# Performance work log

Hardware: AMD Instinct MI355X
Metric: run time of the kernel (lower is better)

Reference implementation:

```python
import jax, jax.numpy as jnp
import numpy as np

B, T, D = 4, 2048, 512
H, HS = 8, 64            # n_head, head_size
E, K = 8, 2              # num_experts, top_k
CAP = int(B * T * K / E * 1.0)  # expert capacity = 2048
EPS = 1e-5


def setup_inputs() -> dict:
    key = jax.random.key(0)
    ks = jax.random.split(key, 16)
    s = lambda k, shp, fan: jax.random.normal(k, shp, jnp.float32) * (fan ** -0.5)
    return {
        "x": jax.random.normal(ks[0], (B, T, D), jnp.float32),
        "ln1_g": jnp.ones((D,), jnp.float32), "ln1_b": jnp.zeros((D,), jnp.float32),
        "Wq": s(ks[1], (H, D, HS), D), "Wk": s(ks[2], (H, D, HS), D), "Wv": s(ks[3], (H, D, HS), D),
        "Wo": s(ks[4], (D, D), D), "bo": jnp.zeros((D,), jnp.float32),
        "ln2_g": jnp.ones((D,), jnp.float32), "ln2_b": jnp.zeros((D,), jnp.float32),
        "Wg": s(ks[5], (D, E), D), "bg": jnp.zeros((E,), jnp.float32),
        "Wn": s(ks[6], (D, E), D), "bn": jnp.zeros((E,), jnp.float32),
        "W1": s(ks[7], (E, D, 4 * D), D), "b1": jnp.zeros((E, 4 * D), jnp.float32),
        "W2": s(ks[8], (E, 4 * D, D), 4 * D), "b2": jnp.zeros((E, D), jnp.float32),
    }


def _ln(x, g, b):
    m = jnp.mean(x, -1, keepdims=True)
    v = jnp.var(x, -1, keepdims=True)
    return (x - m) * jax.lax.rsqrt(v + EPS) * g + b


def _attn(h, Wq, Wk, Wv, Wo, bo):
    q = jnp.einsum('btd,hde->bhte', h, Wq)
    k = jnp.einsum('btd,hde->bhte', h, Wk)
    v = jnp.einsum('btd,hde->bhte', h, Wv)
    # NOTE: source scales by C**-0.5 with C = n_embed (not head_size)
    wei = jnp.einsum('bhte,bhse->bhts', q, k) * (D ** -0.5)
    causal = jnp.tril(jnp.ones((T, T), bool))
    wei = jnp.where(causal, wei, -jnp.inf)
    wei = jax.nn.softmax(wei, axis=-1)
    out = jnp.einsum('bhts,bhse->bhte', wei, v)              # [B,H,T,HS]
    out = out.transpose(0, 2, 1, 3).reshape(B, T, D)          # concat heads
    return out @ Wo + bo


def _moe(h, Wg, bg, Wn, bn, W1, b1, W2, b2):
    logits = h @ Wg + bg
    noise_logits = h @ Wn + bn
    noise = jax.random.normal(jax.random.key(42), logits.shape, logits.dtype) * jax.nn.softplus(noise_logits)
    noisy = logits + noise
    vals, idx = jax.lax.top_k(noisy, K)                       # [B,T,K]
    # softmax over -inf-masked sparse logits == softmax over top-k values, scattered
    gates = (jax.nn.softmax(vals, -1)[..., None] * jax.nn.one_hot(idx, E, dtype=h.dtype)).sum(-2)  # [B,T,E]
    flat_x = h.reshape(-1, D)
    flat_g = gates.reshape(-1, E)
    flat_idx = idx.reshape(-1, K)
    N = flat_x.shape[0]
    mask = (flat_idx[None] == jnp.arange(E)[:, None, None]).any(-1)   # [E,N]
    rank = jnp.cumsum(mask, axis=1) - 1
    keep = mask & (rank < CAP)                                 # first CAP tokens per expert
    slot = jnp.where(keep, rank, CAP)
    tok = jnp.arange(N, dtype=jnp.int32)

    def build(s, kp):
        buf = jnp.zeros(CAP + 1, jnp.int32).at[s].set(tok)
        vb = jnp.zeros(CAP + 1, bool).at[s].set(kp)
        return buf[:CAP], vb[:CAP]

    idx_buf, valid = jax.vmap(build)(slot, keep)               # [E,CAP]
    xg = flat_x[idx_buf]                                       # [E,CAP,D]
    mid = jax.nn.relu(jnp.einsum('ecd,edf->ecf', xg, W1) + b1[:, None, :])
    out = jnp.einsum('ecf,efd->ecd', mid, W2) + b2[:, None, :]
    gate_sel = flat_g[idx_buf, jnp.arange(E)[:, None]]         # [E,CAP]
    w = out * (gate_sel * valid.astype(h.dtype))[..., None]
    upd = jnp.zeros_like(flat_x).at[idx_buf.reshape(-1)].add(w.reshape(-1, D))
    return upd.reshape(h.shape)


def reference(x, ln1_g, ln1_b, Wq, Wk, Wv, Wo, bo, ln2_g, ln2_b,
              Wg, bg, Wn, bn, W1, b1, W2, b2):
    x = x + _attn(_ln(x, ln1_g, ln1_b), Wq, Wk, Wv, Wo, bo)
    x = x + _moe(_ln(x, ln2_g, ln2_b), Wg, bg, Wn, bn, W1, b1, W2, b2)
    return x
```

## Files before the change

kernel.cpp:

```cpp
#include <hip/hip_runtime.h>
#include <math.h>

#define TSEQ 2048
#define DD   512
#define NH   8
#define HSZ  64
#define NE   8
#define NTOK 8192
#define CAPK 2048
#define FF   2048

typedef __bf16 bf16x8 __attribute__((ext_vector_type(8)));
typedef float  f32x4  __attribute__((ext_vector_type(4)));
typedef unsigned int u32;
typedef u32 u32x2 __attribute__((ext_vector_type(2)));
typedef short s16x4 __attribute__((ext_vector_type(4)));

#define WAITVM(N) asm volatile("s_waitcnt vmcnt(" #N ")" ::: "memory")

__device__ __forceinline__ void gload16(const void* g, void* l){
  __builtin_amdgcn_global_load_lds((const __attribute__((address_space(1))) u32*)g,
                                   (__attribute__((address_space(3))) u32*)l, 16, 0, 0);
}

__device__ __forceinline__ u32 pkbf(float a, float b){
  unsigned short ua = __builtin_bit_cast(unsigned short, (__bf16)a);
  unsigned short ub = __builtin_bit_cast(unsigned short, (__bf16)b);
  return (u32)ua | ((u32)ub << 16);
}

__device__ __forceinline__ s16x4 mk4(u32 a, u32 b){
  u32x2 t; t[0] = a; t[1] = b;
  return __builtin_bit_cast(s16x4, t);
}

__device__ __forceinline__ unsigned rotl32(unsigned x, int r){ return (x<<r)|(x>>(32-r)); }

__device__ __forceinline__ void threefry2x32(unsigned c0, unsigned c1, unsigned &o0, unsigned &o1){
  const unsigned k0 = 0u, k1 = 42u;
  const unsigned k2 = k0 ^ k1 ^ 0x1BD11BDAu;
  unsigned x0 = c0 + k0, x1 = c1 + k1;
#define TFR(rot) { x0 += x1; x1 = rotl32(x1, rot); x1 ^= x0; }
  TFR(13) TFR(15) TFR(26) TFR(6)   x0 += k1; x1 += k2 + 1u;
  TFR(17) TFR(29) TFR(16) TFR(24)  x0 += k2; x1 += k0 + 2u;
  TFR(13) TFR(15) TFR(26) TFR(6)   x0 += k0; x1 += k1 + 3u;
  TFR(17) TFR(29) TFR(16) TFR(24)  x0 += k1; x1 += k2 + 4u;
  TFR(13) TFR(15) TFR(26) TFR(6)   x0 += k2; x1 += k0 + 5u;
#undef TFR
  o0 = x0; o1 = x1;
}

__device__ __forceinline__ float erfinv_f(float x){
  float w = -log1pf(-x*x);
  float p;
  if (w < 5.0f){
    w -= 2.5f;
    p = 2.81022636e-08f;
    p = fmaf(p,w, 3.43273939e-07f);
    p = fmaf(p,w,-3.5233877e-06f);
    p = fmaf(p,w,-4.39150654e-06f);
    p = fmaf(p,w, 0.00021858087f);
    p = fmaf(p,w,-0.00125372503f);
    p = fmaf(p,w,-0.00417768164f);
    p = fmaf(p,w, 0.246640727f);
    p = fmaf(p,w, 1.50140941f);
  } else {
    w = sqrtf(w) - 3.0f;
    p = -0.000200214257f;
    p = fmaf(p,w, 0.000100950558f);
    p = fmaf(p,w, 0.00134934322f);
    p = fmaf(p,w,-0.00367342844f);
    p = fmaf(p,w, 0.00573950773f);
    p = fmaf(p,w,-0.0076224613f);
    p = fmaf(p,w, 0.00943887047f);
    p = fmaf(p,w, 1.00167406f);
    p = fmaf(p,w, 2.83297682f);
  }
  return p * x;
}

__global__ __launch_bounds__(256) void prep_kernel(
    const float* __restrict__ x, const float* __restrict__ ln1g, const float* __restrict__ ln1b,
    __bf16* __restrict__ h1hi, __bf16* __restrict__ h1lo,
    const float* __restrict__ Wq, const float* __restrict__ Wk, const float* __restrict__ Wv,
    __bf16* __restrict__ Bqh, __bf16* __restrict__ Bql,
    const float* __restrict__ Wo, __bf16* __restrict__ WoTh, __bf16* __restrict__ WoTl)
{
  __shared__ float t[64][65];
  int blk = blockIdx.x;
  int tid = threadIdx.x;
  if (blk < 2048){
    int row  = blk*4 + (tid >> 6);
    int lane = tid & 63;
    const float* xr = x + (size_t)row*DD;
    float4 a = *(const float4*)(xr + lane*4);
    float4 c = *(const float4*)(xr + 256 + lane*4);
    float s  = a.x+a.y+a.z+a.w + c.x+c.y+c.z+c.w;
    float ss = a.x*a.x+a.y*a.y+a.z*a.z+a.w*a.w + c.x*c.x+c.y*c.y+c.z*c.z+c.w*c.w;
    #pragma unroll
    for (int off = 32; off; off >>= 1){ s += __shfl_xor(s, off); ss += __shfl_xor(ss, off); }
    float m   = s * (1.0f/DD);
    float var = ss * (1.0f/DD) - m*m;
    float r   = 1.0f / sqrtf(var + 1e-5f);
    float4 g1 = *(const float4*)(ln1g + lane*4);
    float4 b1 = *(const float4*)(ln1b + lane*4);
    float4 g2 = *(const float4*)(ln1g + 256 + lane*4);
    float4 b2 = *(const float4*)(ln1b + 256 + lane*4);
    float f1[4], f2[4];
    f1[0]=(a.x-m)*r*g1.x+b1.x; f1[1]=(a.y-m)*r*g1.y+b1.y; f1[2]=(a.z-m)*r*g1.z+b1.z; f1[3]=(a.w-m)*r*g1.w+b1.w;
    f2[0]=(c.x-m)*r*g2.x+b2.x; f2[1]=(c.y-m)*r*g2.y+b2.y; f2[2]=(c.z-m)*r*g2.z+b2.z; f2[3]=(c.w-m)*r*g2.w+b2.w;
    __bf16 h1v[4] __attribute__((aligned(8))), l1v[4] __attribute__((aligned(8)));
    __bf16 h2v[4] __attribute__((aligned(8))), l2v[4] __attribute__((aligned(8)));
    #pragma unroll
    for (int j = 0; j < 4; ++j){
      __bf16 hb = (__bf16)f1[j]; h1v[j]=hb; l1v[j]=(__bf16)(f1[j]-(float)hb);
      __bf16 hc = (__bf16)f2[j]; h2v[j]=hc; l2v[j]=(__bf16)(f2[j]-(float)hc);
    }
    size_t base = (size_t)row*DD + lane*4;
    *(uint2*)(h1hi + base)       = *(const uint2*)h1v;
    *(uint2*)(h1lo + base)       = *(const uint2*)l1v;
    *(uint2*)(h1hi + base + 256) = *(const uint2*)h2v;
    *(uint2*)(h1lo + base + 256) = *(const uint2*)l2v;
  } else if (blk < 2240){
    int bx = blk - 2048;
    int kt = (bx & 7) * 64;
    int z  = bx >> 3;
    int sel = z >> 3, hh = z & 7;
    const float* W = (sel==0 ? Wq : (sel==1 ? Wk : Wv)) + (size_t)hh*DD*HSZ;
    int r = tid>>2, c0 = (tid&3)*16;
    #pragma unroll
    for (int j = 0; j < 16; j += 4){
      float4 v = *(const float4*)&W[(size_t)(kt+r)*HSZ + c0 + j];
      t[r][c0+j]=v.x; t[r][c0+j+1]=v.y; t[r][c0+j+2]=v.z; t[r][c0+j+3]=v.w;
    }
    __syncthreads();
    __bf16 hb[16] __attribute__((aligned(32)));
    __bf16 lb[16] __attribute__((aligned(32)));
    #pragma unroll
    for (int j = 0; j < 16; ++j){
      float f = t[c0+j][r];
      __bf16 h = (__bf16)f; hb[j]=h; lb[j]=(__bf16)(f-(float)h);
    }
    size_t off = (size_t)(z*64 + r)*512 + kt + c0;
    *(uint4*)(Bqh+off) = ((const uint4*)hb)[0]; *(uint4*)(Bqh+off+8) = ((const uint4*)hb)[1];
    *(uint4*)(Bql+off) = ((const uint4*)lb)[0]; *(uint4*)(Bql+off+8) = ((const uint4*)lb)[1];
  } else {
    int bx = blk - 2240;
    int nt = (bx & 7) * 64, mt = (bx >> 3) * 64;
    int r = tid>>2, c0 = (tid&3)*16;
    #pragma unroll
    for (int j = 0; j < 16; j += 4){
      float4 v = *(const float4*)&Wo[(size_t)(mt+r)*DD + nt + c0 + j];
      t[r][c0+j]=v.x; t[r][c0+j+1]=v.y; t[r][c0+j+2]=v.z; t[r][c0+j+3]=v.w;
    }
    __syncthreads();
    __bf16 hb[16] __attribute__((aligned(32)));
    __bf16 lb[16] __attribute__((aligned(32)));
    #pragma unroll
    for (int j = 0; j < 16; ++j){
      float f = t[c0+j][r];
      __bf16 h = (__bf16)f; hb[j]=h; lb[j]=(__bf16)(f-(float)h);
    }
    size_t off = (size_t)(nt + r)*DD + mt + c0;
    *(uint4*)(WoTh+off) = ((const uint4*)hb)[0]; *(uint4*)(WoTh+off+8) = ((const uint4*)hb)[1];
    *(uint4*)(WoTl+off) = ((const uint4*)lb)[0]; *(uint4*)(WoTl+off+8) = ((const uint4*)lb)[1];
  }
}

template<int BIAS, int RES>
__global__ __launch_bounds__(256) void gemm_mfma3(
    const __bf16* __restrict__ Ahi, const __bf16* __restrict__ Alo,
    const __bf16* __restrict__ Bhi, const __bf16* __restrict__ Blo,
    const float* __restrict__ bias, const float* __restrict__ res,
    float* __restrict__ C, int M, int N, int K)
{
  __shared__ __bf16 AsH[2][4096];
  __shared__ __bf16 AsL[2][4096];
  __shared__ __bf16 BsH[2][4096];
  __shared__ __bf16 BsL[2][4096];
  int m0 = blockIdx.y*128, n0 = blockIdx.x*128;
  int tid = threadIdx.x;
  int w = tid>>6, l = tid&63;
  int wm = w>>1, wn = w&1;
  int srow = w*32 + (l>>2);
  int skb  = (l&3)<<4;
  const char* agh = (const char*)(Ahi + (size_t)(m0+srow)*K) + skb;
  const char* agl = (const char*)(Alo + (size_t)(m0+srow)*K) + skb;
  const char* bgh = (const char*)(Bhi + (size_t)(n0+srow)*K) + skb;
  const char* bgl = (const char*)(Blo + (size_t)(n0+srow)*K) + skb;
  size_t r16 = (size_t)16*K*sizeof(__bf16);

  f32x4 acc[4][4] = {};
  int rl = l & 15, kh = l >> 4;
  const __bf16* abh = &AsH[0][(wm*64 + rl)*32 + kh*8];
  const __bf16* abl = &AsL[0][(wm*64 + rl)*32 + kh*8];
  const __bf16* bbh = &BsH[0][(wn*64 + rl)*32 + kh*8];
  const __bf16* bbl = &BsL[0][(wn*64 + rl)*32 + kh*8];

  auto STAGE = [&](int bb, int kt){
    size_t o = (size_t)kt*64;
    gload16(agh+o,     &AsH[bb][w*1024]);
    gload16(agh+o+r16, &AsH[bb][w*1024+512]);
    gload16(agl+o,     &AsL[bb][w*1024]);
    gload16(agl+o+r16, &AsL[bb][w*1024+512]);
    gload16(bgh+o,     &BsH[bb][w*1024]);
    gload16(bgh+o+r16, &BsH[bb][w*1024+512]);
    gload16(bgl+o,     &BsL[bb][w*1024]);
    gload16(bgl+o+r16, &BsL[bb][w*1024+512]);
  };

  int nkt = K >> 5;
  STAGE(0, 0);
  for (int kt = 0; kt < nkt; ++kt){
    int bb = kt & 1;
    if (kt + 1 < nkt){ STAGE(bb^1, kt+1); WAITVM(8); }
    else             { WAITVM(0); }
    __builtin_amdgcn_s_barrier();
    bf16x8 afh[4], afl[4], bfh[4], bfl[4];
    #pragma unroll
    for (int i = 0; i < 4; ++i){
      afh[i] = *(const bf16x8*)(abh + bb*4096 + i*512);
      afl[i] = *(const bf16x8*)(abl + bb*4096 + i*512);
      bfh[i] = *(const bf16x8*)(bbh + bb*4096 + i*512);
      bfl[i] = *(const bf16x8*)(bbl + bb*4096 + i*512);
    }
    #pragma unroll
    for (int fm = 0; fm < 4; ++fm)
      #pragma unroll
      for (int fn = 0; fn < 4; ++fn){
        acc[fm][fn] = __builtin_amdgcn_mfma_f32_16x16x32_bf16(afh[fm], bfl[fn], acc[fm][fn], 0, 0, 0);
        acc[fm][fn] = __builtin_amdgcn_mfma_f32_16x16x32_bf16(afl[fm], bfh[fn], acc[fm][fn], 0, 0, 0);
        acc[fm][fn] = __builtin_amdgcn_mfma_f32_16x16x32_bf16(afh[fm], bfh[fn], acc[fm][fn], 0, 0, 0);
      }
    __builtin_amdgcn_s_barrier();
  }

  int ccol = l & 15, cr = (l >> 4) * 4;
  #pragma unroll
  for (int fn = 0; fn < 4; ++fn){
    int n = n0 + wn*64 + fn*16 + ccol;
    float bv = BIAS ? bias[n] : 0.0f;
    #pragma unroll
    for (int fm = 0; fm < 4; ++fm){
      int mb = m0 + wm*64 + fm*16 + cr;
      #pragma unroll
      for (int r = 0; r < 4; ++r){
        float v = acc[fm][fn][r] + bv;
        if (RES) v += res[(size_t)(mb+r)*N + n];
        C[(size_t)(mb+r)*N + n] = v;
      }
    }
  }
}

template<int STORE_BF16, int RELU, int GATHER, int LOGN, int EBITS>
__global__ __launch_bounds__(256) void gemm_mfma(
    const __bf16* __restrict__ A, const __bf16* __restrict__ Bt,
    const float* __restrict__ bias, void* __restrict__ Cv,
    const int* __restrict__ idxb, int M, int N, int K)
{
  __shared__ __bf16 Asl[2][4096];
  __shared__ __bf16 Bsl[2][4096];
  int flat = blockIdx.x;
  int e = flat & ((1<<EBITS)-1);
  int tile = flat >> EBITS;
  int n0 = (tile & ((1<<LOGN)-1)) * 128;
  int m0 = (tile >> LOGN) * 128;
  const __bf16* Be = Bt + (size_t)e*N*K;
  const float*  be = bias + (size_t)e*N;
  int tid = threadIdx.x;
  int w = tid>>6, l = tid&63;
  int wm = w>>1, wn = w&1;
  int srow = w*32 + (l>>2);
  int skb  = (l&3)<<4;
  const char* ag;
  if (GATHER){
    int tok = idxb[e*CAPK + m0 + srow];
    ag = (const char*)(A + (size_t)tok*K) + skb;
  } else {
    ag = (const char*)(A + (size_t)e*M*K + (size_t)(m0 + srow)*K) + skb;
  }
  const char* bg = (const char*)(Be + (size_t)(n0 + srow)*K) + skb;
  size_t r16;
  if (GATHER){
    int tok2 = idxb[e*CAPK + m0 + srow + 16];
    r16 = (size_t)((const char*)(A + (size_t)tok2*K) + skb - ag);
  } else {
    r16 = (size_t)16*K*sizeof(__bf16);
  }

  f32x4 acc[4][4] = {};
  int rl = l & 15, kh = l >> 4;
  const __bf16* abase = &Asl[0][(wm*64 + rl)*32 + kh*8];
  const __bf16* bbase = &Bsl[0][(wn*64 + rl)*32 + kh*8];

  size_t br16 = (size_t)16*K*sizeof(__bf16);
  auto STAGE = [&](int bb, int kt){
    size_t o = (size_t)kt*64;
    gload16(ag+o,      &Asl[bb][w*1024]);
    gload16(ag+o+r16,  &Asl[bb][w*1024+512]);
    gload16(bg+o,      &Bsl[bb][w*1024]);
    gload16(bg+o+br16, &Bsl[bb][w*1024+512]);
  };

  int nkt = K >> 5;
  STAGE(0, 0);
  for (int kt = 0; kt < nkt; ++kt){
    int bb = kt & 1;
    if (kt + 1 < nkt){ STAGE(bb^1, kt+1); WAITVM(4); }
    else             { WAITVM(0); }
    __builtin_amdgcn_s_barrier();
    bf16x8 af[4], bf[4];
    #pragma unroll
    for (int i = 0; i < 4; ++i){
      af[i] = *(const bf16x8*)(abase + bb*4096 + i*512);
      bf[i] = *(const bf16x8*)(bbase + bb*4096 + i*512);
    }
    #pragma unroll
    for (int fm = 0; fm < 4; ++fm)
      #pragma unroll
      for (int fn = 0; fn < 4; ++fn)
        acc[fm][fn] = __builtin_amdgcn_mfma_f32_16x16x32_bf16(af[fm], bf[fn], acc[fm][fn], 0, 0, 0);
    __builtin_amdgcn_s_barrier();
  }

  int ccol = l & 15, cr = (l >> 4) * 4;
  char* Ce = (char*)Cv + (size_t)e*M*N*(STORE_BF16 ? 2 : 4);
  #pragma unroll
  for (int fn = 0; fn < 4; ++fn){
    int n = n0 + wn*64 + fn*16 + ccol;
    float bv = be[n];
    #pragma unroll
    for (int fm = 0; fm < 4; ++fm){
      int mb = m0 + wm*64 + fm*16 + cr;
      #pragma unroll
      for (int r = 0; r < 4; ++r){
        float v = acc[fm][fn][r] + bv;
        if (RELU) v = fmaxf(v, 0.f);
        if (STORE_BF16) ((__bf16*)Ce)[(size_t)(mb+r)*N + n] = (__bf16)v;
        else            ((float*)Ce)[(size_t)(mb+r)*N + n] = v;
      }
    }
  }
}

__global__ __launch_bounds__(256) void transp_conv2(const float* __restrict__ W1,
    const float* __restrict__ W2, __bf16* __restrict__ d1, __bf16* __restrict__ d2)
{
  __shared__ __bf16 t[64][72];
  int e = blockIdx.z;
  int id = blockIdx.x;
  const float* s; __bf16* d; int Ms, Ns, mt, nt;
  if (id < 256){ s = W1; d = d1; Ms = DD; Ns = FF; nt = (id&31)*64; mt = (id>>5)*64; }
  else { int i2 = id-256; s = W2; d = d2; Ms = FF; Ns = DD; nt = (i2&7)*64; mt = (i2>>3)*64; }
  s += (size_t)e*Ms*Ns;
  d += (size_t)e*Ms*Ns;
  int tid = threadIdx.x;
  int r = tid>>2, c0 = (tid&3)*16;
  #pragma unroll
  for (int j = 0; j < 16; j += 4){
    float4 v = *(const float4*)&s[(size_t)(mt+r)*Ns + nt + c0 + j];
    t[r][c0+j]   = (__bf16)v.x; t[r][c0+j+1] = (__bf16)v.y;
    t[r][c0+j+2] = (__bf16)v.z; t[r][c0+j+3] = (__bf16)v.w;
  }
  __syncthreads();
  __bf16 tmp[16] __attribute__((aligned(32)));
  #pragma unroll
  for (int j = 0; j < 16; ++j) tmp[j] = t[c0+j][r];
  uint4* dp = (uint4*)&d[(size_t)(nt+r)*Ms + mt + c0];
  dp[0] = ((const uint4*)tmp)[0];
  dp[1] = ((const uint4*)tmp)[1];
}

__global__ __launch_bounds__(256) void convert_kv(const float* __restrict__ qkv,
    __bf16* __restrict__ khi, __bf16* __restrict__ klo,
    __bf16* __restrict__ vthi, __bf16* __restrict__ vtlo)
{
  int t0 = blockIdx.x*64;
  int bh = blockIdx.y;
  int b = bh >> 3, h = bh & 7;
  int tid = threadIdx.x;
  {
    int r = tid >> 2, e0 = (tid & 3) * 16;
    const float* src = qkv + ((size_t)(b*TSEQ + t0 + r))*1536 + 512 + h*64 + e0;
    __bf16 hi[16] __attribute__((aligned(16)));
    __bf16 lo[16] __attribute__((aligned(16)));
    #pragma unroll
    for (int j = 0; j < 16; j += 4){
      float4 v = *(const float4*)(src + j);
      float f[4] = {v.x, v.y, v.z, v.w};
      #pragma unroll
      for (int q = 0; q < 4; ++q){
        __bf16 hb = (__bf16)f[q];
        hi[j+q] = hb; lo[j+q] = (__bf16)(f[q] - (float)hb);
      }
    }
    size_t off = ((size_t)(bh*TSEQ + t0 + r))*64 + e0;
    *(uint4*)(khi + off)     = ((const uint4*)hi)[0];
    *(uint4*)(khi + off + 8) = ((const uint4*)hi)[1];
    *(uint4*)(klo + off)     = ((const uint4*)lo)[0];
    *(uint4*)(klo + off + 8) = ((const uint4*)lo)[1];
  }
  {
    int key0 = (tid & 15) * 4, e0 = (tid >> 4) * 4;
    float4 v[4];
    #pragma unroll
    for (int j = 0; j < 4; ++j)
      v[j] = *(const float4*)(qkv + ((size_t)(b*TSEQ + t0 + key0 + j))*1536 + 1024 + h*64 + e0);
    float col[4][4];
    col[0][0]=v[0].x; col[0][1]=v[1].x; col[0][2]=v[2].x; col[0][3]=v[3].x;
    col[1][0]=v[0].y; col[1][1]=v[1].y; col[1][2]=v[2].y; col[1][3]=v[3].y;
    col[2][0]=v[0].z; col[2][1]=v[1].z; col[2][2]=v[2].z; col[2][3]=v[3].z;
    col[3][0]=v[0].w; col[3][1]=v[1].w; col[3][2]=v[2].w; col[3][3]=v[3].w;
    #pragma unroll
    for (int kk = 0; kk < 4; ++kk){
      __bf16 hi[4] __attribute__((aligned(8)));
      __bf16 lo[4] __attribute__((aligned(8)));
      #pragma unroll
      for (int j = 0; j < 4; ++j){
        __bf16 hb = (__bf16)col[kk][j];
        hi[j] = hb; lo[j] = (__bf16)(col[kk][j] - (float)hb);
      }
      size_t off = ((size_t)(bh*64 + e0 + kk))*TSEQ + t0 + key0;
      *(uint2*)(vthi + off) = *(const uint2*)hi;
      *(uint2*)(vtlo + off) = *(const uint2*)lo;
    }
  }
}

__global__ __launch_bounds__(512) void attn_mfma(const float* __restrict__ qkv,
    const __bf16* __restrict__ khi_g, const __bf16* __restrict__ klo_g,
    const __bf16* __restrict__ vthi_g, const __bf16* __restrict__ vtlo_g,
    __bf16* __restrict__ ahi, __bf16* __restrict__ alo)
{
  extern __shared__ __align__(16) char ldsbuf[];
  int bh = blockIdx.x;
  int qtA = blockIdx.y, qtB = 15 - qtA;
  int b = bh >> 3, h = bh & 7;
  int tid = threadIdx.x;
  int w = tid >> 6, l = tid & 63;
  int g = l >> 4, r = l & 15;
  const float qsc = 0.04419417382415922f * 1.4426950408889634f;

  int qb[2]; qb[0] = qtA*128 + w*16; qb[1] = qtB*128 + (7-w)*16;
  int kdiag[2]; kdiag[0] = qtA; kdiag[1] = qtB;

  bf16x8 qhi[2][2], qlo[2][2];
  #pragma unroll
  for (int qf = 0; qf < 2; ++qf)
    #pragma unroll
    for (int ks = 0; ks < 2; ++ks){
      const float* src = qkv + ((size_t)(b*TSEQ + qb[qf] + r))*1536 + h*64 + ks*32 + g*8;
      float4 v0 = *(const float4*)src;
      float4 v1 = *(const float4*)(src + 4);
      float f[8] = {v0.x,v0.y,v0.z,v0.w,v1.x,v1.y,v1.z,v1.w};
      bf16x8 hi, lo;
      #pragma unroll
      for (int i = 0; i < 8; ++i){
        float fs = f[i] * qsc;
        __bf16 hb = (__bf16)fs;
        hi[i] = hb; lo[i] = (__bf16)(fs - (float)hb);
      }
      qhi[qf][ks] = hi; qlo[qf][ks] = lo;
    }

  f32x4 ot[4][2] = {};
  float m_r[2] = {-INFINITY, -INFINITY};
  float l_r[2] = {0.f, 0.f};

  int nkt = qtB + 1;
  size_t kbase = (size_t)bh*TSEQ*64;
  size_t vbase = (size_t)bh*64*TSEQ;

  auto STAGE = [&](int buf, int kt){
    int row = tid >> 3, cc = tid & 7;
    char* base = ldsbuf + buf*65536 + (w << 10);
    #pragma unroll
    for (int p = 0; p < 2; ++p){
      int krow = p*64 + row;
      int ksw = (cc ^ (krow & 7)) * 8;
      gload16(khi_g + kbase + (size_t)(kt*128 + krow)*64 + ksw, base + p*8192);
      gload16(klo_g + kbase + (size_t)(kt*128 + krow)*64 + ksw, base + 16384 + p*8192);
      int vch = p*8 + cc;
      int vsw = ((vch ^ (row & 7)) & 15) * 8;
      gload16(vthi_g + vbase + (size_t)row*TSEQ + kt*128 + vsw, base + 32768 + p*8192);
      gload16(vtlo_g + vbase + (size_t)row*TSEQ + kt*128 + vsw, base + 49152 + p*8192);
    }
  };

  STAGE(0, 0);

  for (int kt = 0; kt < nkt; ++kt){
    int buf = kt & 1;
    if (kt + 1 < nkt){ STAGE(buf ^ 1, kt + 1); WAITVM(8); }
    else             { WAITVM(0); }
    __builtin_amdgcn_s_barrier();

    bool act[2];
    act[0] = (kt <= kdiag[0]);
    act[1] = true;

    const char* K0 = ldsbuf + buf*65536;
    const char* K1 = K0 + 16384;
    const char* V0 = K0 + 32768;
    const char* V1 = K0 + 49152;

    f32x4 s[8][2] = {};
    #pragma unroll
    for (int kf = 0; kf < 8; ++kf){
      int rowk = kf*16 + r;
      int rsw = (rowk & 7) << 4;
      #pragma unroll
      for (int ks = 0; ks < 2; ++ks){
        int off = rowk*128 + ((((ks*4 + g) << 4)) ^ rsw);
        bf16x8 khf = *(const bf16x8*)(K0 + off);
        bf16x8 klf = *(const bf16x8*)(K1 + off);
        #pragma unroll
        for (int qf = 0; qf < 2; ++qf){
          if (act[qf]){
            s[kf][qf] = __builtin_amdgcn_mfma_f32_16x16x32_bf16(khf, qlo[qf][ks], s[kf][qf], 0,0,0);
            s[kf][qf] = __builtin_amdgcn_mfma_f32_16x16x32_bf16(klf, qhi[qf][ks], s[kf][qf], 0,0,0);
            s[kf][qf] = __builtin_amdgcn_mfma_f32_16x16x32_bf16(khf, qhi[qf][ks], s[kf][qf], 0,0,0);
          }
        }
      }
    }

    #pragma unroll
    for (int qf = 0; qf < 2; ++qf){
      if (act[qf]){
        int q = qb[qf] + r;
        float mx = -INFINITY;
        if (kt == kdiag[qf]){
          #pragma unroll
          for (int kf = 0; kf < 8; ++kf)
            #pragma unroll
            for (int e = 0; e < 4; ++e){
              int key = kt*128 + kf*16 + g*4 + e;
              float sv = (key <= q) ? s[kf][qf][e] : -INFINITY;
              s[kf][qf][e] = sv;
              mx = fmaxf(mx, sv);
            }
        } else {
          #pragma unroll
          for (int kf = 0; kf < 8; ++kf)
            #pragma unroll
            for (int e = 0; e < 4; ++e)
              mx = fmaxf(mx, s[kf][qf][e]);
        }
        mx = fmaxf(mx, __shfl_xor(mx, 16));
        mx = fmaxf(mx, __shfl_xor(mx, 32));
        if (__any(mx > m_r[qf])){
          float mn = fmaxf(m_r[qf], mx);
          float fj = exp2f(m_r[qf] - mn);
          m_r[qf] = mn;
          l_r[qf] *= fj;
          #pragma unroll
          for (int ef = 0; ef < 4; ++ef)
            #pragma unroll
            for (int e = 0; e < 4; ++e)
              ot[ef][qf][e] *= fj;
        }
        float ts = 0.f;
        #pragma unroll
        for (int kf = 0; kf < 8; ++kf)
          #pragma unroll
          for (int e = 0; e < 4; ++e){
            float pv = exp2f(s[kf][qf][e] - m_r[qf]);
            s[kf][qf][e] = pv; ts += pv;
          }
        ts += __shfl_xor(ts, 16); ts += __shfl_xor(ts, 32);
        l_r[qf] += ts;
      }
    }

    #pragma unroll
    for (int kf = 0; kf < 8; ++kf){
      u32 PH[2][2], PL[2][2];
      #pragma unroll
      for (int qf = 0; qf < 2; ++qf){
        if (act[qf]){
          float p0 = s[kf][qf][0], p1 = s[kf][qf][1], p2 = s[kf][qf][2], p3 = s[kf][qf][3];
          __bf16 h0=(__bf16)p0, h1=(__bf16)p1, h2=(__bf16)p2, h3=(__bf16)p3;
          PH[qf][0] = pkbf(p0, p1);
          PH[qf][1] = pkbf(p2, p3);
          PL[qf][0] = pkbf(p0-(float)h0, p1-(float)h1);
          PL[qf][1] = pkbf(p2-(float)h2, p3-(float)h3);
        }
      }
      int chunk = 2*kf + (g>>1);
      int pb = (chunk >> 3) << 13;
      int cl = chunk & 7;
      #pragma unroll
      for (int ef = 0; ef < 4; ++ef){
        int rowv = ef*16 + r;
        int off = pb + rowv*128 + ((cl ^ (rowv & 7)) << 4) + (g&1)*8;
        s16x4 vh = *(const s16x4*)(V0 + off);
        s16x4 vl = *(const s16x4*)(V1 + off);
        #pragma unroll
        for (int qf = 0; qf < 2; ++qf){
          if (act[qf]){
            s16x4 ph = mk4(PH[qf][0], PH[qf][1]);
            s16x4 pl = mk4(PL[qf][0], PL[qf][1]);
            ot[ef][qf] = __builtin_amdgcn_mfma_f32_16x16x16bf16_1k(vh, pl, ot[ef][qf], 0,0,0);
            ot[ef][qf] = __builtin_amdgcn_mfma_f32_16x16x16bf16_1k(vl, ph, ot[ef][qf], 0,0,0);
            ot[ef][qf] = __builtin_amdgcn_mfma_f32_16x16x16bf16_1k(vh, ph, ot[ef][qf], 0,0,0);
          }
        }
      }
    }
    __builtin_amdgcn_s_barrier();
  }

  float* Osh = (float*)ldsbuf;
  #pragma unroll
  for (int qf = 0; qf < 2; ++qf){
    float inv = 1.0f / l_r[qf];
    int qloc = (qf ? (7-w) : w)*16 + r;
    #pragma unroll
    for (int ef = 0; ef < 4; ++ef)
      #pragma unroll
      for (int e = 0; e < 4; ++e)
        Osh[qloc*68 + ef*16 + g*4 + e] = ot[ef][qf][e] * inv;
    __syncthreads();
    {
      int qt = qf ? qtB : qtA;
      int q = tid >> 2, e0 = (tid & 3)*16;
      const float* srow = Osh + q*68 + e0;
      size_t base = ((size_t)(b*TSEQ + qt*128 + q))*DD + h*64 + e0;
      #pragma unroll
      for (int j = 0; j < 4; ++j){
        float4 v = *(const float4*)(srow + j*4);
        float f[4] = {v.x, v.y, v.z, v.w};
        __bf16 hb[4] __attribute__((aligned(8)));
        __bf16 lb[4] __attribute__((aligned(8)));
        #pragma unroll
        for (int q2 = 0; q2 < 4; ++q2){
          __bf16 h2b = (__bf16)f[q2];
          hb[q2] = h2b; lb[q2] = (__bf16)(f[q2] - (float)h2b);
        }
        *(uint2*)(ahi + base + j*4) = *(const uint2*)hb;
        *(uint2*)(alo + base + j*4) = *(const uint2*)lb;
      }
    }
    __syncthreads();
  }
}

__global__ __launch_bounds__(256) void routerln_kernel(const float* __restrict__ x1,
    const float* __restrict__ gw, const float* __restrict__ bw,
    const float* __restrict__ Wg, const float* __restrict__ bg,
    const float* __restrict__ Wn, const float* __restrict__ bn,
    __bf16* __restrict__ h2b,
    int* __restrict__ idx0, int* __restrict__ idx1,
    float* __restrict__ g0, float* __restrict__ g1)
{
  int wid = threadIdx.x >> 6, lane = threadIdx.x & 63;
  int tok = blockIdx.x*4 + wid;
  const float* xr = x1 + (size_t)tok*DD;
  float4 a = *(const float4*)(xr + lane*4);
  float4 c = *(const float4*)(xr + 256 + lane*4);
  float s  = a.x+a.y+a.z+a.w + c.x+c.y+c.z+c.w;
  float ss = a.x*a.x+a.y*a.y+a.z*a.z+a.w*a.w + c.x*c.x+c.y*c.y+c.z*c.z+c.w*c.w;
  #pragma unroll
  for (int off = 32; off; off >>= 1){ s += __shfl_xor(s, off); ss += __shfl_xor(ss, off); }
  float m   = s * (1.0f/DD);
  float var = ss * (1.0f/DD) - m*m;
  float rr  = 1.0f / sqrtf(var + 1e-5f);
  float4 g1v = *(const float4*)(gw + lane*4);
  float4 b1v = *(const float4*)(bw + lane*4);
  float4 g2v = *(const float4*)(gw + 256 + lane*4);
  float4 b2v = *(const float4*)(bw + 256 + lane*4);
  float f1[4], f2[4];
  f1[0]=(a.x-m)*rr*g1v.x+b1v.x; f1[1]=(a.y-m)*rr*g1v.y+b1v.y; f1[2]=(a.z-m)*rr*g1v.z+b1v.z; f1[3]=(a.w-m)*rr*g1v.w+b1v.w;
  f2[0]=(c.x-m)*rr*g2v.x+b2v.x; f2[1]=(c.y-m)*rr*g2v.y+b2v.y; f2[2]=(c.z-m)*rr*g2v.z+b2v.z; f2[3]=(c.w-m)*rr*g2v.w+b2v.w;
  {
    __bf16 h1v[4] __attribute__((aligned(8)));
    __bf16 h2v[4] __attribute__((aligned(8)));
    #pragma unroll
    for (int j = 0; j < 4; ++j){ h1v[j] = (__bf16)f1[j]; h2v[j] = (__bf16)f2[j]; }
    size_t base = (size_t)tok*DD + lane*4;
    *(uint2*)(h2b + base)       = *(const uint2*)h1v;
    *(uint2*)(h2b + base + 256) = *(const uint2*)h2v;
  }
  float ag[8] = {0,0,0,0,0,0,0,0}, an[8] = {0,0,0,0,0,0,0,0};
  int d1 = lane*4, d2 = 256 + lane*4;
  #pragma unroll
  for (int j = 0; j < 4; ++j){
    const float* wg1 = Wg + (size_t)(d1+j)*8;
    const float* wn1 = Wn + (size_t)(d1+j)*8;
    const float* wg2 = Wg + (size_t)(d2+j)*8;
    const float* wn2 = Wn + (size_t)(d2+j)*8;
    #pragma unroll
    for (int e = 0; e < 8; ++e){
      ag[e] = fmaf(f1[j], wg1[e], ag[e]); an[e] = fmaf(f1[j], wn1[e], an[e]);
      ag[e] = fmaf(f2[j], wg2[e], ag[e]); an[e] = fmaf(f2[j], wn2[e], an[e]);
    }
  }
  #pragma unroll
  for (int off = 32; off; off >>= 1){
    #pragma unroll
    for (int e = 0; e < 8; ++e){ ag[e] += __shfl_xor(ag[e], off); an[e] += __shfl_xor(an[e], off); }
  }
  __shared__ float ns[4][8];
  if (lane < 8){
    int e = lane;
    float lg = ag[e] + bg[e];
    float nl = an[e] + bn[e];
    float sp = fmaxf(nl, 0.f) + log1pf(expf(-fabsf(nl)));
    unsigned i = (unsigned)(tok*8 + e);
    unsigned r0b, r1b;
    threefry2x32(0u, i, r0b, r1b);
    unsigned bits = r0b ^ r1b;
    float f = __uint_as_float((bits >> 9) | 0x3f800000u) - 1.0f;
    float u = fmaf(f, 2.0f, -0.99999994f);
    u = fmaxf(u, -0.99999994f);
    float z = 1.41421356f * erfinv_f(u);
    ns[wid][e] = lg + z*sp;
  }
  __syncthreads();
  if (lane == 0){
    float v0 = -INFINITY; int i0 = 0;
    #pragma unroll
    for (int e = 0; e < 8; ++e){ float v = ns[wid][e]; if (v > v0){ v0 = v; i0 = e; } }
    float v1 = -INFINITY; int i1 = 0;
    #pragma unroll
    for (int e = 0; e < 8; ++e){ if (e != i0){ float v = ns[wid][e]; if (v > v1){ v1 = v; i1 = e; } } }
    float dexp = expf(v1 - v0);
    float ssum = 1.0f + dexp;
    idx0[tok] = i0; idx1[tok] = i1;
    g0[tok] = 1.0f/ssum; g1[tok] = dexp/ssum;
  }
}

__global__ __launch_bounds__(256) void route_scan(const int* __restrict__ idx0,
    const int* __restrict__ idx1, int* __restrict__ idx_buf, int* __restrict__ tok_slot)
{
  int e = blockIdx.x, tid = threadIdx.x;
  for (int i = tid; i < CAPK; i += 256) idx_buf[e*CAPK + i] = 0;
  __syncthreads();
  int base = tid * 32;
  int cnt = 0;
  for (int j = 0; j < 32; ++j){ int t = base + j; cnt += (idx0[t]==e || idx1[t]==e) ? 1 : 0; }
  __shared__ int ps[256];
  ps[tid] = cnt; __syncthreads();
  for (int off = 1; off < 256; off <<= 1){
    int add = (tid >= off) ? ps[tid - off] : 0;
    __syncthreads();
    ps[tid] += add;
    __syncthreads();
  }
  int slot = ps[tid] - cnt;
  for (int j = 0; j < 32; ++j){
    int t = base + j;
    int k = (idx0[t]==e) ? 0 : ((idx1[t]==e) ? 1 : -1);
    if (k >= 0){
      if (slot < CAPK){ idx_buf[e*CAPK + slot] = t; tok_slot[t*2 + k] = slot; }
      else            { tok_slot[t*2 + k] = -1; }
      slot++;
    }
  }
}

__global__ __launch_bounds__(128) void combine_kernel(const float* __restrict__ x1,
    const __bf16* __restrict__ eout, const int* __restrict__ idx0, const int* __restrict__ idx1,
    const float* __restrict__ g0, const float* __restrict__ g1,
    const int* __restrict__ tok_slot, float* __restrict__ outp)
{
  int n = blockIdx.x, t = threadIdx.x;
  float4 acc = *(const float4*)(x1 + (size_t)n*DD + t*4);
  #pragma unroll
  for (int k = 0; k < 2; ++k){
    int s = tok_slot[n*2 + k];
    if (s >= 0){
      int e  = (k==0) ? idx0[n] : idx1[n];
      float g = (k==0) ? g0[n] : g1[n];
      __bf16 vb[4] __attribute__((aligned(8)));
      *(uint2*)vb = *(const uint2*)(eout + ((size_t)(e*CAPK + s))*DD + t*4);
      acc.x = fmaf(g, (float)vb[0], acc.x); acc.y = fmaf(g, (float)vb[1], acc.y);
      acc.z = fmaf(g, (float)vb[2], acc.z); acc.w = fmaf(g, (float)vb[3], acc.w);
    }
  }
  *(float4*)(outp + (size_t)n*DD + t*4) = acc;
}

extern "C" void kernel_launch(void* const* d_in, const int* in_sizes, int n_in,
                              void* d_out, int out_size, void* d_ws, size_t ws_size,
                              hipStream_t stream)
{
  const float* x    = (const float*)d_in[0];
  const float* ln1g = (const float*)d_in[1];
  const float* ln1b = (const float*)d_in[2];
  const float* Wq   = (const float*)d_in[3];
  const float* Wk   = (const float*)d_in[4];
  const float* Wv   = (const float*)d_in[5];
  const float* Wo   = (const float*)d_in[6];
  const float* bo   = (const float*)d_in[7];
  const float* ln2g = (const float*)d_in[8];
  const float* ln2b = (const float*)d_in[9];
  const float* Wg   = (const float*)d_in[10];
  const float* bg   = (const float*)d_in[11];
  const float* Wn   = (const float*)d_in[12];
  const float* bn   = (const float*)d_in[13];
  const float* W1   = (const float*)d_in[14];
  const float* b1   = (const float*)d_in[15];
  const float* W2   = (const float*)d_in[16];
  const float* b2   = (const float*)d_in[17];
  float* out = (float*)d_out;
  char* ws = (char*)d_ws;
  const size_t MB = 1u << 20;

  (void)hipFuncSetAttribute((const void*)attn_mfma,
      hipFuncAttributeMaxDynamicSharedMemorySize, 131072);

  __bf16* h1hi   = (__bf16*)(ws);
  __bf16* h1lo   = (__bf16*)(ws + 8*MB);
  __bf16* attnhi = (__bf16*)(ws);
  __bf16* attnlo = (__bf16*)(ws + 8*MB);
  __bf16* h2b    = (__bf16*)(ws);
  float*  qkv    = (float*)(ws + 16*MB);
  __bf16* W1T    = (__bf16*)(ws + 16*MB);
  __bf16* W2T    = (__bf16*)(ws + 32*MB);
  __bf16* eoutb  = (__bf16*)(ws + 48*MB);
  float*  x1     = (float*)(ws + 64*MB);
  __bf16* Khi    = (__bf16*)(ws + 80*MB);
  __bf16* Klo    = (__bf16*)(ws + 88*MB);
  __bf16* Vthi   = (__bf16*)(ws + 96*MB);
  __bf16* Vtlo   = (__bf16*)(ws + 104*MB);
  __bf16* Bqh    = (__bf16*)(ws + 80*MB);
  __bf16* Bql    = (__bf16*)(ws + 82*MB);
  __bf16* mid    = (__bf16*)(ws + 80*MB);
  __bf16* WoTh   = (__bf16*)(ws + 144*MB);
  __bf16* WoTl   = (__bf16*)(ws + 144*MB + 512*1024);
  char*   smallp = ws + 145*MB;
  int*   idx0     = (int*)smallp;
  int*   idx1     = idx0 + NTOK;
  float* g0       = (float*)(idx1 + NTOK);
  float* g1       = g0 + NTOK;
  int*   tok_slot = (int*)(g1 + NTOK);
  int*   idx_buf  = tok_slot + NTOK*2;

  prep_kernel<<<dim3(2304), 256, 0, stream>>>(x, ln1g, ln1b, h1hi, h1lo,
      Wq, Wk, Wv, Bqh, Bql, Wo, WoTh, WoTl);
  gemm_mfma3<0,0><<<dim3(12,64), 256, 0, stream>>>(h1hi, h1lo, Bqh, Bql, nullptr, nullptr, qkv, NTOK, 1536, DD);
  convert_kv<<<dim3(TSEQ/64, 32), 256, 0, stream>>>(qkv, Khi, Klo, Vthi, Vtlo);
  attn_mfma<<<dim3(32, 8), 512, 131072, stream>>>(qkv, Khi, Klo, Vthi, Vtlo, attnhi, attnlo);
  gemm_mfma3<1,1><<<dim3(4,64), 256, 0, stream>>>(attnhi, attnlo, WoTh, WoTl, bo, x, x1, NTOK, DD, DD);
  routerln_kernel<<<dim3(NTOK/4), 256, 0, stream>>>(x1, ln2g, ln2b, Wg, bg, Wn, bn,
      h2b, idx0, idx1, g0, g1);
  transp_conv2<<<dim3(512,1,NE), 256, 0, stream>>>(W1, W2, W1T, W2T);
  route_scan<<<dim3(NE), 256, 0, stream>>>(idx0, idx1, idx_buf, tok_slot);
  gemm_mfma<1,1,1,4,3><<<dim3(8*16*16), 256, 0, stream>>>(
      h2b, W1T, b1, mid, idx_buf, CAPK, FF, DD);
  gemm_mfma<1,0,0,2,3><<<dim3(8*16*4), 256, 0, stream>>>(
      mid, W2T, b2, eoutb, nullptr, CAPK, DD, FF);
  combine_kernel<<<dim3(NTOK), 128, 0, stream>>>(x1, eoutb, idx0, idx1, g0, g1, tok_slot, out);
}
```

Before: 367.1 us.

## Fuse QKV split/transposition into GEMM epilogue and drop convert_kv kernel

```diff
diff --git a/kernel.cpp b/kernel.cpp
--- a/kernel.cpp
+++ b/kernel.cpp
@@ -27,6 +27,13 @@
   unsigned short ua = __builtin_bit_cast(unsigned short, (__bf16)a);
   unsigned short ub = __builtin_bit_cast(unsigned short, (__bf16)b);
   return (u32)ua | ((u32)ub << 16);
+}
+
+__device__ __forceinline__ u32 pksplit(float v){
+  __bf16 hb = (__bf16)v;
+  __bf16 lb = (__bf16)(v - (float)hb);
+  return (u32)__builtin_bit_cast(unsigned short, hb) |
+         ((u32)__builtin_bit_cast(unsigned short, lb) << 16);
 }
 
 __device__ __forceinline__ s16x4 mk4(u32 a, u32 b){
@@ -167,18 +174,30 @@
   }
 }
 
-template<int BIAS, int RES>
+template<int MODE, int NN>
 __global__ __launch_bounds__(256) void gemm_mfma3(
     const __bf16* __restrict__ Ahi, const __bf16* __restrict__ Alo,
     const __bf16* __restrict__ Bhi, const __bf16* __restrict__ Blo,
-    const float* __restrict__ bias, const float* __restrict__ res,
-    float* __restrict__ C, int M, int N, int K)
+    const float* __restrict__ bias, const float* __restrict__ res, float* __restrict__ C,
+    __bf16* __restrict__ qh, __bf16* __restrict__ ql,
+    __bf16* __restrict__ kh, __bf16* __restrict__ kl,
+    __bf16* __restrict__ vth, __bf16* __restrict__ vtl,
+    int M, int N, int K)
 {
-  __shared__ __bf16 AsH[2][4096];
-  __shared__ __bf16 AsL[2][4096];
-  __shared__ __bf16 BsH[2][4096];
-  __shared__ __bf16 BsL[2][4096];
-  int m0 = blockIdx.y*128, n0 = blockIdx.x*128;
+  __shared__ __align__(16) char smem[65536];
+  __bf16* AsH = (__bf16*)smem;
+  __bf16* AsL = (__bf16*)(smem + 16384);
+  __bf16* BsH = (__bf16*)(smem + 32768);
+  __bf16* BsL = (__bf16*)(smem + 49152);
+
+  int flat  = blockIdx.x;
+  int chunk = flat / (8*NN);
+  int rem   = flat % (8*NN);
+  int mloc  = rem & 7;
+  int nn    = rem >> 3;
+  int m0 = (chunk*8 + mloc)*128;
+  int n0 = nn*128;
+
   int tid = threadIdx.x;
   int w = tid>>6, l = tid&63;
   int wm = w>>1, wn = w&1;
@@ -191,22 +210,22 @@
   size_t r16 = (size_t)16*K*sizeof(__bf16);
 
   f32x4 acc[4][4] = {};
-  int rl = l & 15, kh = l >> 4;
-  const __bf16* abh = &AsH[0][(wm*64 + rl)*32 + kh*8];
-  const __bf16* abl = &AsL[0][(wm*64 + rl)*32 + kh*8];
-  const __bf16* bbh = &BsH[0][(wn*64 + rl)*32 + kh*8];
-  const __bf16* bbl = &BsL[0][(wn*64 + rl)*32 + kh*8];
+  int rl = l & 15, kh_ = l >> 4;
+  const __bf16* abh = AsH + (wm*64 + rl)*32 + kh_*8;
+  const __bf16* abl = AsL + (wm*64 + rl)*32 + kh_*8;
+  const __bf16* bbh = BsH + (wn*64 + rl)*32 + kh_*8;
+  const __bf16* bbl = BsL + (wn*64 + rl)*32 + kh_*8;
 
   auto STAGE = [&](int bb, int kt){
     size_t o = (size_t)kt*64;
-    gload16(agh+o,     &AsH[bb][w*1024]);
-    gload16(agh+o+r16, &AsH[bb][w*1024+512]);
-    gload16(agl+o,     &AsL[bb][w*1024]);
-    gload16(agl+o+r16, &AsL[bb][w*1024+512]);
-    gload16(bgh+o,     &BsH[bb][w*1024]);
-    gload16(bgh+o+r16, &BsH[bb][w*1024+512]);
-    gload16(bgl+o,     &BsL[bb][w*1024]);
-    gload16(bgl+o+r16, &BsL[bb][w*1024+512]);
+    gload16(agh+o,     AsH + bb*4096 + w*1024);
+    gload16(agh+o+r16, AsH + bb*4096 + w*1024+512);
+    gload16(agl+o,     AsL + bb*4096 + w*1024);
+    gload16(agl+o+r16, AsL + bb*4096 + w*1024+512);
+    gload16(bgh+o,     BsH + bb*4096 + w*1024);
+    gload16(bgh+o+r16, BsH + bb*4096 + w*1024+512);
+    gload16(bgl+o,     BsL + bb*4096 + w*1024);
+    gload16(bgl+o+r16, BsL + bb*4096 + w*1024+512);
   };
 
   int nkt = K >> 5;
@@ -236,18 +255,95 @@
   }
 
   int ccol = l & 15, cr = (l >> 4) * 4;
-  #pragma unroll
-  for (int fn = 0; fn < 4; ++fn){
-    int n = n0 + wn*64 + fn*16 + ccol;
-    float bv = BIAS ? bias[n] : 0.0f;
-    #pragma unroll
-    for (int fm = 0; fm < 4; ++fm){
-      int mb = m0 + wm*64 + fm*16 + cr;
+  if (MODE == 0){
+    #pragma unroll
+    for (int fn = 0; fn < 4; ++fn){
+      int n = n0 + wn*64 + fn*16 + ccol;
+      float bv = bias[n];
       #pragma unroll
-      for (int r = 0; r < 4; ++r){
-        float v = acc[fm][fn][r] + bv;
-        if (RES) v += res[(size_t)(mb+r)*N + n];
-        C[(size_t)(mb+r)*N + n] = v;
+      for (int fm = 0; fm < 4; ++fm){
+        int mb = m0 + wm*64 + fm*16 + cr;
+        #pragma unroll
+        for (int r = 0; r < 4; ++r){
+          float v = acc[fm][fn][r] + bv + res[(size_t)(mb+r)*N + n];
+          C[(size_t)(mb+r)*N + n] = v;
+        }
+      }
+    }
+  } else {
+    u32 (*eps)[132] = (u32(*)[132])smem;
+    int sel = n0 >> 9;
+    int b   = m0 >> 11;
+    int tb  = m0 & 2047;
+    int dbase = n0 & 511;
+    const float qsc = 0.04419417382415922f * 1.4426950408889634f;
+    float sc = (sel == 0) ? qsc : 1.0f;
+    #pragma unroll
+    for (int p = 0; p < 2; ++p){
+      __syncthreads();
+      if (sel < 2){
+        if (wm == p){
+          #pragma unroll
+          for (int fm = 0; fm < 4; ++fm)
+            #pragma unroll
+            for (int fn = 0; fn < 4; ++fn)
+              #pragma unroll
+              for (int r = 0; r < 4; ++r)
+                eps[fm*16 + cr + r][wn*64 + fn*16 + ccol] = pksplit(acc[fm][fn][r] * sc);
+        }
+        __syncthreads();
+        int row = tid >> 2, q4 = tid & 3;
+        int hh = (dbase >> 6) + (q4 >> 1);
+        int e0 = (q4 & 1) * 32;
+        const u32* src = &eps[row][q4*32];
+        __bf16 hbuf[32] __attribute__((aligned(16)));
+        __bf16 lbuf[32] __attribute__((aligned(16)));
+        #pragma unroll
+        for (int j = 0; j < 32; ++j){
+          u32 pk = src[j];
+          hbuf[j] = __builtin_bit_cast(__bf16, (unsigned short)(pk & 0xffffu));
+          lbuf[j] = __builtin_bit_cast(__bf16, (unsigned short)(pk >> 16));
+        }
+        size_t off = ((size_t)(b*8 + hh)*TSEQ + tb + p*64 + row)*64 + e0;
+        __bf16* dh = sel ? kh : qh;
+        __bf16* dl = sel ? kl : ql;
+        #pragma unroll
+        for (int j = 0; j < 4; ++j){
+          *(uint4*)(dh + off + j*8) = ((const uint4*)hbuf)[j];
+          *(uint4*)(dl + off + j*8) = ((const uint4*)lbuf)[j];
+        }
+      } else {
+        if (wn == p){
+          #pragma unroll
+          for (int fn = 0; fn < 4; ++fn)
+            #pragma unroll
+            for (int fm = 0; fm < 4; ++fm){
+              u32 pk4[4] __attribute__((aligned(16)));
+              #pragma unroll
+              for (int r = 0; r < 4; ++r)
+                pk4[r] = pksplit(acc[fm][fn][r]);
+              *(uint4*)&eps[fn*16 + ccol][wm*64 + fm*16 + cr] = *(const uint4*)pk4;
+            }
+        }
+        __syncthreads();
+        int col = tid >> 2, tq = tid & 3;
+        int d = dbase + p*64 + col;
+        int hh = d >> 6, e = d & 63;
+        const u32* src = &eps[col][tq*32];
+        __bf16 hbuf[32] __attribute__((aligned(16)));
+        __bf16 lbuf[32] __attribute__((aligned(16)));
+        #pragma unroll
+        for (int j = 0; j < 32; ++j){
+          u32 pk = src[j];
+          hbuf[j] = __builtin_bit_cast(__bf16, (unsigned short)(pk & 0xffffu));
+          lbuf[j] = __builtin_bit_cast(__bf16, (unsigned short)(pk >> 16));
+        }
+        size_t off = ((size_t)(b*8 + hh)*64 + e)*TSEQ + tb + tq*32;
+        #pragma unroll
+        for (int j = 0; j < 4; ++j){
+          *(uint4*)(vth + off + j*8) = ((const uint4*)hbuf)[j];
+          *(uint4*)(vtl + off + j*8) = ((const uint4*)lbuf)[j];
+        }
       }
     }
   }
@@ -372,63 +468,8 @@
   dp[1] = ((const uint4*)tmp)[1];
 }
 
-__global__ __launch_bounds__(256) void convert_kv(const float* __restrict__ qkv,
-    __bf16* __restrict__ khi, __bf16* __restrict__ klo,
-    __bf16* __restrict__ vthi, __bf16* __restrict__ vtlo)
-{
-  int t0 = blockIdx.x*64;
-  int bh = blockIdx.y;
-  int b = bh >> 3, h = bh & 7;
-  int tid = threadIdx.x;
-  {
-    int r = tid >> 2, e0 = (tid & 3) * 16;
-    const float* src = qkv + ((size_t)(b*TSEQ + t0 + r))*1536 + 512 + h*64 + e0;
-    __bf16 hi[16] __attribute__((aligned(16)));
-    __bf16 lo[16] __attribute__((aligned(16)));
-    #pragma unroll
-    for (int j = 0; j < 16; j += 4){
-      float4 v = *(const float4*)(src + j);
-      float f[4] = {v.x, v.y, v.z, v.w};
-      #pragma unroll
-      for (int q = 0; q < 4; ++q){
-        __bf16 hb = (__bf16)f[q];
-        hi[j+q] = hb; lo[j+q] = (__bf16)(f[q] - (float)hb);
-      }
-    }
-    size_t off = ((size_t)(bh*TSEQ + t0 + r))*64 + e0;
-    *(uint4*)(khi + off)     = ((const uint4*)hi)[0];
-    *(uint4*)(khi + off + 8) = ((const uint4*)hi)[1];
-    *(uint4*)(klo + off)     = ((const uint4*)lo)[0];
-    *(uint4*)(klo + off + 8) = ((const uint4*)lo)[1];
-  }
-  {
-    int key0 = (tid & 15) * 4, e0 = (tid >> 4) * 4;
-    float4 v[4];
-    #pragma unroll
-    for (int j = 0; j < 4; ++j)
-      v[j] = *(const float4*)(qkv + ((size_t)(b*TSEQ + t0 + key0 + j))*1536 + 1024 + h*64 + e0);
-    float col[4][4];
-    col[0][0]=v[0].x; col[0][1]=v[1].x; col[0][2]=v[2].x; col[0][3]=v[3].x;
-    col[1][0]=v[0].y; col[1][1]=v[1].y; col[1][2]=v[2].y; col[1][3]=v[3].y;
-    col[2][0]=v[0].z; col[2][1]=v[1].z; col[2][2]=v[2].z; col[2][3]=v[3].z;
-    col[3][0]=v[0].w; col[3][1]=v[1].w; col[3][2]=v[2].w; col[3][3]=v[3].w;
-    #pragma unroll
-    for (int kk = 0; kk < 4; ++kk){
-      __bf16 hi[4] __attribute__((aligned(8)));
-      __bf16 lo[4] __attribute__((aligned(8)));
-      #pragma unroll
-      for (int j = 0; j < 4; ++j){
-        __bf16 hb = (__bf16)col[kk][j];
-        hi[j] = hb; lo[j] = (__bf16)(col[kk][j] - (float)hb);
-      }
-      size_t off = ((size_t)(bh*64 + e0 + kk))*TSEQ + t0 + key0;
-      *(uint2*)(vthi + off) = *(const uint2*)hi;
-      *(uint2*)(vtlo + off) = *(const uint2*)lo;
-    }
-  }
-}
-
-__global__ __launch_bounds__(512) void attn_mfma(const float* __restrict__ qkv,
+__global__ __launch_bounds__(512) void attn_mfma(
+    const __bf16* __restrict__ qhi_g, const __bf16* __restrict__ qlo_g,
     const __bf16* __restrict__ khi_g, const __bf16* __restrict__ klo_g,
     const __bf16* __restrict__ vthi_g, const __bf16* __restrict__ vtlo_g,
     __bf16* __restrict__ ahi, __bf16* __restrict__ alo)
@@ -440,7 +481,6 @@
   int tid = threadIdx.x;
   int w = tid >> 6, l = tid & 63;
   int g = l >> 4, r = l & 15;
-  const float qsc = 0.04419417382415922f * 1.4426950408889634f;
 
   int qb[2]; qb[0] = qtA*128 + w*16; qb[1] = qtB*128 + (7-w)*16;
   int kdiag[2]; kdiag[0] = qtA; kdiag[1] = qtB;
@@ -450,18 +490,9 @@
   for (int qf = 0; qf < 2; ++qf)
     #pragma unroll
     for (int ks = 0; ks < 2; ++ks){
-      const float* src = qkv + ((size_t)(b*TSEQ + qb[qf] + r))*1536 + h*64 + ks*32 + g*8;
-      float4 v0 = *(const float4*)src;
-      float4 v1 = *(const float4*)(src + 4);
-      float f[8] = {v0.x,v0.y,v0.z,v0.w,v1.x,v1.y,v1.z,v1.w};
-      bf16x8 hi, lo;
-      #pragma unroll
-      for (int i = 0; i < 8; ++i){
-        float fs = f[i] * qsc;
-        __bf16 hb = (__bf16)fs;
-        hi[i] = hb; lo[i] = (__bf16)(fs - (float)hb);
-      }
-      qhi[qf][ks] = hi; qlo[qf][ks] = lo;
+      size_t qoff = ((size_t)bh*TSEQ + qb[qf] + r)*64 + ks*32 + g*8;
+      qhi[qf][ks] = *(const bf16x8*)(qhi_g + qoff);
+      qlo[qf][ks] = *(const bf16x8*)(qlo_g + qoff);
     }
 
   f32x4 ot[4][2] = {};
@@ -818,15 +849,16 @@
   __bf16* attnhi = (__bf16*)(ws);
   __bf16* attnlo = (__bf16*)(ws + 8*MB);
   __bf16* h2b    = (__bf16*)(ws);
-  float*  qkv    = (float*)(ws + 16*MB);
+  __bf16* Qhi    = (__bf16*)(ws + 16*MB);
+  __bf16* Qlo    = (__bf16*)(ws + 24*MB);
+  __bf16* Khi    = (__bf16*)(ws + 32*MB);
+  __bf16* Klo    = (__bf16*)(ws + 40*MB);
+  __bf16* Vthi   = (__bf16*)(ws + 48*MB);
+  __bf16* Vtlo   = (__bf16*)(ws + 56*MB);
   __bf16* W1T    = (__bf16*)(ws + 16*MB);
   __bf16* W2T    = (__bf16*)(ws + 32*MB);
   __bf16* eoutb  = (__bf16*)(ws + 48*MB);
   float*  x1     = (float*)(ws + 64*MB);
-  __bf16* Khi    = (__bf16*)(ws + 80*MB);
-  __bf16* Klo    = (__bf16*)(ws + 88*MB);
-  __bf16* Vthi   = (__bf16*)(ws + 96*MB);
-  __bf16* Vtlo   = (__bf16*)(ws + 104*MB);
   __bf16* Bqh    = (__bf16*)(ws + 80*MB);
   __bf16* Bql    = (__bf16*)(ws + 82*MB);
   __bf16* mid    = (__bf16*)(ws + 80*MB);
@@ -842,10 +874,11 @@
 
   prep_kernel<<<dim3(2304), 256, 0, stream>>>(x, ln1g, ln1b, h1hi, h1lo,
       Wq, Wk, Wv, Bqh, Bql, Wo, WoTh, WoTl);
-  gemm_mfma3<0,0><<<dim3(12,64), 256, 0, stream>>>(h1hi, h1lo, Bqh, Bql, nullptr, nullptr, qkv, NTOK, 1536, DD);
-  convert_kv<<<dim3(TSEQ/64, 32), 256, 0, stream>>>(qkv, Khi, Klo, Vthi, Vtlo);
-  attn_mfma<<<dim3(32, 8), 512, 131072, stream>>>(qkv, Khi, Klo, Vthi, Vtlo, attnhi, attnlo);
-  gemm_mfma3<1,1><<<dim3(4,64), 256, 0, stream>>>(attnhi, attnlo, WoTh, WoTl, bo, x, x1, NTOK, DD, DD);
+  gemm_mfma3<1,12><<<dim3(64*12), 256, 0, stream>>>(h1hi, h1lo, Bqh, Bql,
+      nullptr, nullptr, nullptr, Qhi, Qlo, Khi, Klo, Vthi, Vtlo, NTOK, 1536, DD);
+  attn_mfma<<<dim3(32, 8), 512, 131072, stream>>>(Qhi, Qlo, Khi, Klo, Vthi, Vtlo, attnhi, attnlo);
+  gemm_mfma3<0,4><<<dim3(64*4), 256, 0, stream>>>(attnhi, attnlo, WoTh, WoTl,
+      bo, x, x1, nullptr, nullptr, nullptr, nullptr, nullptr, nullptr, NTOK, DD, DD);
   routerln_kernel<<<dim3(NTOK/4), 256, 0, stream>>>(x1, ln2g, ln2b, Wg, bg, Wn, bn,
       h2b, idx0, idx1, g0, g1);
   transp_conv2<<<dim3(512,1,NE), 256, 0, stream>>>(W1, W2, W1T, W2T);
```

After: 362.9 us. No clear change (-1.1%).
